# Optimization experiments

Measured on AMD Instinct MI355X. Metric: run time of the kernel, lower is better.

The kernel has to match this reference:

```python
import jax, jax.numpy as jnp
import numpy as np

N = 65536   # total nodes
E = 1048576 # total edges (avg degree 16)
B = 512     # graphs in batch
H = 4       # gat1 heads
C = 64      # per-head channels / GNN_HIDDEN


def segment_softmax(logits, seg, num_segments):
    # numerically stable softmax over segments (PyG softmax semantics, eps=1e-16)
    m = jax.ops.segment_max(logits, seg, num_segments=num_segments)
    m = jnp.where(jnp.isfinite(m), m, 0.0)
    e = jnp.exp(logits - m[seg])
    s = jax.ops.segment_sum(e, seg, num_segments=num_segments)
    return e / (s[seg] + 1e-16)


def gat_conv(x, edge_index, edge_attr, W, att_src, att_dst, We, att_edge, bias, heads, out_ch, concat):
    # PyG GATConv with edge_dim, add_self_loops=False
    n = x.shape[0]
    h = (x @ W).reshape(n, heads, out_ch)                 # (N,H,C)
    src, dst = edge_index[0], edge_index[1]
    a_s = jnp.sum(h * att_src, axis=-1)                   # (N,H)
    a_d = jnp.sum(h * att_dst, axis=-1)                   # (N,H)
    he = (edge_attr @ We).reshape(-1, heads, out_ch)      # (E,H,C)
    a_e = jnp.sum(he * att_edge, axis=-1)                 # (E,H)
    alpha = jax.nn.leaky_relu(a_s[src] + a_d[dst] + a_e, negative_slope=0.2)
    alpha = segment_softmax(alpha, dst, n)                # softmax over incoming edges per dst
    out = jax.ops.segment_sum(h[src] * alpha[..., None], dst, num_segments=n)  # (N,H,C)
    out = out.reshape(n, heads * out_ch) if concat else out.mean(axis=1)
    return out + bias


def setup_inputs() -> dict:
    key = jax.random.key(0)
    ks = jax.random.split(key, 24)
    s = 0.05
    d = {}
    d["global_feat"] = jax.random.normal(ks[0], (B, 512), jnp.float32)
    d["x"] = jax.random.normal(ks[1], (N, 13), jnp.float32)
    d["roi_feats"] = jax.random.normal(ks[2], (N, 256), jnp.float32)
    d["edge_index"] = jax.random.randint(ks[3], (2, E), 0, N)
    d["edge_attr"] = jax.random.normal(ks[4], (E, 5), jnp.float32)
    d["batch_vec"] = jnp.sort(jax.random.randint(ks[5], (N,), 0, B))
    # roi_proj / scene_proj
    d["roi_W"] = jax.random.normal(ks[6], (256, 64), jnp.float32) * s
    d["roi_b"] = jnp.zeros((64,), jnp.float32)
    d["scene_W"] = jax.random.normal(ks[7], (512, 128), jnp.float32) * s
    d["scene_b"] = jnp.zeros((128,), jnp.float32)
    d["g1_W"] = jax.random.normal(ks[8], (77, H * C), jnp.float32) * s
    d["g1_att_src"] = jax.random.normal(ks[9], (H, C), jnp.float32) * s
    d["g1_att_dst"] = jax.random.normal(ks[10], (H, C), jnp.float32) * s
    d["g1_We"] = jax.random.normal(ks[11], (5, H * C), jnp.float32) * s
    d["g1_att_edge"] = jax.random.normal(ks[12], (H, C), jnp.float32) * s
    d["g1_bias"] = jnp.zeros((H * C,), jnp.float32)
    # gat2: 256 -> 64, 1 head
    d["g2_W"] = jax.random.normal(ks[13], (H * C, C), jnp.float32) * s
    d["g2_att_src"] = jax.random.normal(ks[14], (1, C), jnp.float32) * s
    d["g2_att_dst"] = jax.random.normal(ks[15], (1, C), jnp.float32) * s
    d["g2_We"] = jax.random.normal(ks[16], (5, C), jnp.float32) * s
    d["g2_att_edge"] = jax.random.normal(ks[17], (1, C), jnp.float32) * s
    d["g2_bias"] = jnp.zeros((C,), jnp.float32)
    # attention pooling gate + classifier
    d["gate_W"] = jax.random.normal(ks[18], (C, 1), jnp.float32) * s
    d["gate_b"] = jnp.zeros((1,), jnp.float32)
    d["cls1_W"] = jax.random.normal(ks[19], (128 + C, 64), jnp.float32) * s
    d["cls1_b"] = jnp.zeros((64,), jnp.float32)
    d["cls2_W"] = jax.random.normal(ks[20], (64, 3), jnp.float32) * s
    d["cls2_b"] = jnp.zeros((3,), jnp.float32)
    return d


def reference(global_feat, x, roi_feats, edge_index, edge_attr, batch_vec,
              roi_W, roi_b, scene_W, scene_b,
              g1_W, g1_att_src, g1_att_dst, g1_We, g1_att_edge, g1_bias,
              g2_W, g2_att_src, g2_att_dst, g2_We, g2_att_edge, g2_bias,
              gate_W, gate_b, cls1_W, cls1_b, cls2_W, cls2_b):
    scene = global_feat @ scene_W + scene_b                       # (B,128)
    vis = jax.nn.relu(roi_feats @ roi_W + roi_b)                  # (N,64)
    h = jnp.concatenate([x, vis], axis=-1)                        # (N,77)
    h = jax.nn.relu(gat_conv(h, edge_index, edge_attr, g1_W, g1_att_src, g1_att_dst, g1_We, g1_att_edge, g1_bias, H, C, True))
    h = gat_conv(h, edge_index, edge_attr, g2_W, g2_att_src, g2_att_dst, g2_We, g2_att_edge, g2_bias, 1, C, False)  # (N,64)
    # GlobalAttention pooling
    gate = segment_softmax((h @ gate_W + gate_b)[:, 0], batch_vec, B)
    rel = jax.ops.segment_sum(gate[:, None] * h, batch_vec, num_segments=B)  # (B,64)
    comb = jnp.concatenate([scene, rel], axis=-1)                 # (B,192)
    hid = jax.nn.relu(comb @ cls1_W + cls1_b)                     # dropout off (eval)
    return hid @ cls2_W + cls2_b                                  # (B,3)
```

## Files before the change

kernel.cpp:

```cpp
#include <hip/hip_runtime.h>

#define N_NODES 65536
#define N_EDGES 1048576
#define NB      512

typedef unsigned short u16;
typedef unsigned int   u32;
typedef unsigned long long u64;

typedef __attribute__((ext_vector_type(8))) short bf16x8;
typedef __attribute__((ext_vector_type(4))) float f32x4;

__device__ __forceinline__ float bf2f(u16 u) { return __uint_as_float(((u32)u) << 16); }
__device__ __forceinline__ float lo16(u32 u) { return __uint_as_float(u << 16); }
__device__ __forceinline__ float hi16(u32 u) { return __uint_as_float(u & 0xffff0000u); }
__device__ __forceinline__ u16 f2bf(float f) {
    u32 u = __float_as_uint(f);
    u32 r = (u + 0x7fffu + ((u >> 16) & 1u)) >> 16;
    return (u16)r;
}
__device__ __forceinline__ u32 pk2(float a, float b) {
    return (u32)f2bf(a) | ((u32)f2bf(b) << 16);
}
__device__ __forceinline__ float wsum(float v) {
    for (int o = 32; o; o >>= 1) v += __shfl_xor(v, o, 64);
    return v;
}
__device__ __forceinline__ float wmax(float v) {
    for (int o = 32; o; o >>= 1) v = fmaxf(v, __shfl_xor(v, o, 64));
    return v;
}

__global__ __launch_bounds__(512) void k_wprep(const float* __restrict__ g1W, const float* __restrict__ roiW,
                                               const float* __restrict__ g2W,
                                               const float* __restrict__ g1We, const float* __restrict__ g1ae,
                                               const float* __restrict__ g2We, const float* __restrict__ g2ae,
                                               u16* __restrict__ g1Wt, u16* __restrict__ roiWt,
                                               u16* __restrict__ g2Wt, float* __restrict__ M1,
                                               float* __restrict__ M2) {
    int b = blockIdx.x, t = threadIdx.x;
    if (b < 48) {
        int idx = b * 512 + t;
        int c = idx / 96, k = idx - 96 * c;
        float v = 0.f;
        if (k < 77) {
            int ko = (k < 64) ? (13 + k) : (k - 64);
            v = g1W[(size_t)ko * 256 + c];
        }
        g1Wt[idx] = f2bf(v);
    } else if (b < 80) {
        int idx = (b - 48) * 512 + t;
        int c = idx >> 8, k = idx & 255;
        roiWt[idx] = f2bf(roiW[(size_t)k * 64 + c]);
    } else if (b < 112) {
        int idx = (b - 80) * 512 + t;
        int c = idx >> 8, k = idx & 255;
        g2Wt[idx] = f2bf(g2W[(size_t)k * 64 + c]);
    } else {
        if (t < 20) {
            int j = t >> 2, h = t & 3;
            float s = 0.f;
            for (int c = 0; c < 64; c++) s += g1We[j * 256 + h * 64 + c] * g1ae[h * 64 + c];
            M1[t] = s;
        } else if (t < 25) {
            int j = t - 20;
            float s = 0.f;
            for (int c = 0; c < 64; c++) s += g2We[j * 64 + c] * g2ae[c];
            M2[j] = s;
        }
    }
}

__global__ __launch_bounds__(256) void k_scene(const float* __restrict__ gf, const float* __restrict__ W,
                                               const float* __restrict__ bias, float* __restrict__ scene) {
    int idx = blockIdx.x * 256 + threadIdx.x;
    int b = idx >> 7, j = idx & 127;
    float acc = 0.f;
    for (int k = 0; k < 512; k++) acc += gf[b * 512 + k] * W[k * 128 + j];
    scene[idx] = acc + bias[j];
}

__global__ __launch_bounds__(256) void k_hist(const int* ei, int* cnt) {
    int e = blockIdx.x * 256 + threadIdx.x;
    atomicAdd(&cnt[ei[N_EDGES + e]], 1);
}

__global__ __launch_bounds__(256) void k_scan_blk(const int* __restrict__ cnt, int* __restrict__ pre,
                                                  int* __restrict__ bsum) {
    __shared__ int sd[256];
    int t = threadIdx.x, b = blockIdx.x;
    int base = b * 1024 + t * 4;
    int4 c = *(const int4*)(cnt + base);
    int s = c.x + c.y + c.z + c.w;
    sd[t] = s;
    __syncthreads();
    for (int off = 1; off < 256; off <<= 1) {
        int v = (t >= off) ? sd[t - off] : 0;
        __syncthreads();
        sd[t] += v;
        __syncthreads();
    }
    int excl = sd[t] - s;
    int4 p;
    p.x = excl;
    p.y = excl + c.x;
    p.z = excl + c.x + c.y;
    p.w = excl + c.x + c.y + c.z;
    *(int4*)(pre + base) = p;
    if (t == 255) bsum[b] = sd[255];
}

__global__ __launch_bounds__(64) void k_scan_top(int* bsum) {
    int t = threadIdx.x;
    int v = bsum[t];
    int inc = v;
    for (int off = 1; off < 64; off <<= 1) {
        int u = __shfl_up(inc, off, 64);
        if (t >= off) inc += u;
    }
    bsum[t] = inc - v;
}

__global__ __launch_bounds__(256) void k_scan_fix(const int* __restrict__ pre, const int* __restrict__ bsum,
                                                  int* __restrict__ row_ptr, int* __restrict__ coarse_cur) {
    int i = blockIdx.x * 256 + threadIdx.x;
    int v = pre[i] + bsum[i >> 10];
    row_ptr[i] = v;
    if ((i & 255) == 0) coarse_cur[i >> 8] = v;
    if (i == 0) row_ptr[N_NODES] = N_EDGES;
}

__global__ __launch_bounds__(256) void k_bucket(const int* __restrict__ ei, int* coarse_cur,
                                                u32* __restrict__ bpack, int* __restrict__ bsrc) {
    __shared__ u32 stageP[2048];
    __shared__ int stageS[2048];
    __shared__ int bcnt[256], bscan[256], boff[256], gbase[256];
    int t = threadIdx.x;
    int e0 = blockIdx.x * 2048;
    bcnt[t] = 0;
    __syncthreads();
    int dreg[8], sreg[8];
    for (int it = 0; it < 8; it++) {
        int e = e0 + it * 256 + t;
        int dd = ei[N_EDGES + e];
        dreg[it] = dd;
        sreg[it] = ei[e];
        atomicAdd(&bcnt[dd >> 8], 1);
    }
    __syncthreads();
    int v = bcnt[t];
    bscan[t] = v;
    __syncthreads();
    for (int off = 1; off < 256; off <<= 1) {
        int u = (t >= off) ? bscan[t - off] : 0;
        __syncthreads();
        bscan[t] += u;
        __syncthreads();
    }
    boff[t] = bscan[t] - v;
    gbase[t] = v ? atomicAdd(&coarse_cur[t], v) : 0;
    __syncthreads();
    for (int it = 0; it < 8; it++) {
        int e = e0 + it * 256 + t;
        int b = dreg[it] >> 8;
        int pos = atomicAdd(&boff[b], 1);
        stageP[pos] = ((u32)e << 12) | (u32)(dreg[it] & 255);
        stageS[pos] = sreg[it];
    }
    __syncthreads();
    for (int idx = t; idx < 2048; idx += 256) {
        int lo = 0, hi = 255;
        while (lo < hi) { int mid = (lo + hi) >> 1; if (bscan[mid] > idx) hi = mid; else lo = mid + 1; }
        int b = lo;
        int g = gbase[b] + (idx - (bscan[b] - bcnt[b]));
        bpack[g] = stageP[idx];
        bsrc[g] = stageS[idx];
    }
}

__global__ __launch_bounds__(256) void k_sortp(const u32* __restrict__ bpack, const int* __restrict__ bsrc,
                                               const int* __restrict__ row_ptr, const float* __restrict__ ea,
                                               const float* __restrict__ M1, const float* __restrict__ M2,
                                               int* __restrict__ ssrc, float* __restrict__ a1es,
                                               float* __restrict__ a2es) {
    __shared__ int cur[256];
    int t = threadIdx.x, b = blockIdx.x;
    int nbase = b * 256;
    cur[t] = row_ptr[nbase + t];
    __syncthreads();
    float m1[20], m2[5];
    #pragma unroll
    for (int j = 0; j < 20; j++) m1[j] = M1[j];
    #pragma unroll
    for (int j = 0; j < 5; j++) m2[j] = M2[j];
    int beg = row_ptr[nbase];
    int end = row_ptr[nbase + 256];
    for (int i = beg + t; i < end; i += 256) {
        u32 wd = bpack[i];
        int src = bsrc[i];
        int d8 = wd & 255;
        int e = (int)(wd >> 12);
        int pos = atomicAdd(&cur[d8], 1);
        ssrc[pos] = src;
        const float* ep = ea + (size_t)e * 5;
        float v0 = ep[0], v1 = ep[1], v2 = ep[2], v3 = ep[3], v4 = ep[4];
        float4 o;
        o.x = v0*m1[0]  + v1*m1[4]  + v2*m1[8]  + v3*m1[12] + v4*m1[16];
        o.y = v0*m1[1]  + v1*m1[5]  + v2*m1[9]  + v3*m1[13] + v4*m1[17];
        o.z = v0*m1[2]  + v1*m1[6]  + v2*m1[10] + v3*m1[14] + v4*m1[18];
        o.w = v0*m1[3]  + v1*m1[7]  + v2*m1[11] + v3*m1[15] + v4*m1[19];
        *(float4*)(a1es + (size_t)pos * 4) = o;
        a2es[pos] = v0*m2[0] + v1*m2[1] + v2*m2[2] + v3*m2[3] + v4*m2[4];
    }
}

__global__ __launch_bounds__(256) void k_vis(const float* __restrict__ roi, const u16* __restrict__ Wt,
                                             const float* __restrict__ bias, u16* __restrict__ out) {
    __shared__ u16 At[64][264];
    int t = threadIdx.x;
    int w = t >> 6, l = t & 63, lo = l & 15, hi = l >> 4;
    int n0 = blockIdx.x * 64;
    int r = t >> 2, sub = t & 3;
    const float* rp = roi + (size_t)(n0 + r) * 256 + sub * 4;
    #pragma unroll
    for (int q = 0; q < 16; q++) {
        float4 v = *(const float4*)(rp + q * 16);
        uint2 p;
        p.x = pk2(v.x, v.y);
        p.y = pk2(v.z, v.w);
        *(uint2*)&At[r][q * 16 + sub * 4] = p;
    }
    float bb[4][4];
    #pragma unroll
    for (int cb = 0; cb < 4; cb++)
        #pragma unroll
        for (int rg = 0; rg < 4; rg++) bb[cb][rg] = bias[cb * 16 + hi * 4 + rg];
    __syncthreads();
    f32x4 acc[4];
    #pragma unroll
    for (int cb = 0; cb < 4; cb++) acc[cb] = (f32x4){0.f, 0.f, 0.f, 0.f};
    #pragma unroll
    for (int ks = 0; ks < 8; ks++) {
        bf16x8 af = *(const bf16x8*)(&At[w * 16 + lo][ks * 32 + hi * 8]);
        #pragma unroll
        for (int cb = 0; cb < 4; cb++) {
            bf16x8 wf = *(const bf16x8*)(Wt + (size_t)(cb * 16 + lo) * 256 + ks * 32 + hi * 8);
            acc[cb] = __builtin_amdgcn_mfma_f32_16x16x32_bf16(wf, af, acc[cb], 0, 0, 0);
        }
    }
    int nrow = n0 + w * 16 + lo;
    #pragma unroll
    for (int cb = 0; cb < 4; cb++) {
        uint2 p;
        p.x = pk2(fmaxf(acc[cb][0] + bb[cb][0], 0.f), fmaxf(acc[cb][1] + bb[cb][1], 0.f));
        p.y = pk2(fmaxf(acc[cb][2] + bb[cb][2], 0.f), fmaxf(acc[cb][3] + bb[cb][3], 0.f));
        *(uint2*)(out + (size_t)nrow * 64 + cb * 16 + hi * 4) = p;
    }
}

__global__ __launch_bounds__(256) void k_h1(const float* __restrict__ x, const u16* __restrict__ vis,
                                            const u16* __restrict__ Wt,
                                            const float* __restrict__ as_, const float* __restrict__ ad_,
                                            u16* __restrict__ h1, float* __restrict__ a1s,
                                            float* __restrict__ a1d) {
    __shared__ u16 At[64][104];
    int t = threadIdx.x;
    int w = t >> 6, l = t & 63, lo = l & 15, hi = l >> 4;
    int n0 = blockIdx.x * 64;
    int r = t >> 2, sub = t & 3;
    {
        const uint4* vp = (const uint4*)(vis + (size_t)(n0 + r) * 64 + sub * 16);
        uint4 v0 = vp[0], v1 = vp[1];
        *(uint4*)&At[r][sub * 16] = v0;
        *(uint4*)&At[r][sub * 16 + 8] = v1;
        if (sub == 0) {
            const float* xp = x + (size_t)(n0 + r) * 13;
            #pragma unroll
            for (int j = 0; j < 13; j++) At[r][64 + j] = f2bf(xp[j]);
        } else if (sub == 1) {
            #pragma unroll
            for (int j = 77; j < 96; j++) At[r][j] = 0;
        }
    }
    bf16x8 wf[4][3];
    float asv[4][4], adv[4][4];
    #pragma unroll
    for (int cb = 0; cb < 4; cb++) {
        #pragma unroll
        for (int ks = 0; ks < 3; ks++)
            wf[cb][ks] = *(const bf16x8*)(Wt + (size_t)(w * 64 + cb * 16 + lo) * 96 + ks * 32 + hi * 8);
        #pragma unroll
        for (int rg = 0; rg < 4; rg++) {
            asv[cb][rg] = as_[w * 64 + cb * 16 + hi * 4 + rg];
            adv[cb][rg] = ad_[w * 64 + cb * 16 + hi * 4 + rg];
        }
    }
    __syncthreads();
    #pragma unroll
    for (int nb = 0; nb < 4; nb++) {
        f32x4 acc[4];
        #pragma unroll
        for (int cb = 0; cb < 4; cb++) acc[cb] = (f32x4){0.f, 0.f, 0.f, 0.f};
        #pragma unroll
        for (int ks = 0; ks < 3; ks++) {
            bf16x8 af = *(const bf16x8*)(&At[nb * 16 + lo][ks * 32 + hi * 8]);
            #pragma unroll
            for (int cb = 0; cb < 4; cb++)
                acc[cb] = __builtin_amdgcn_mfma_f32_16x16x32_bf16(wf[cb][ks], af, acc[cb], 0, 0, 0);
        }
        int nrow = n0 + nb * 16 + lo;
        float ps = 0.f, pd = 0.f;
        #pragma unroll
        for (int cb = 0; cb < 4; cb++) {
            uint2 p;
            p.x = pk2(acc[cb][0], acc[cb][1]);
            p.y = pk2(acc[cb][2], acc[cb][3]);
            *(uint2*)(h1 + (size_t)nrow * 256 + w * 64 + cb * 16 + hi * 4) = p;
            ps += acc[cb][0] * asv[cb][0] + acc[cb][1] * asv[cb][1]
                + acc[cb][2] * asv[cb][2] + acc[cb][3] * asv[cb][3];
            pd += acc[cb][0] * adv[cb][0] + acc[cb][1] * adv[cb][1]
                + acc[cb][2] * adv[cb][2] + acc[cb][3] * adv[cb][3];
        }
        ps += __shfl_xor(ps, 16, 64); ps += __shfl_xor(ps, 32, 64);
        pd += __shfl_xor(pd, 16, 64); pd += __shfl_xor(pd, 32, 64);
        if (hi == 0) {
            a1s[nrow * 4 + w] = ps;
            a1d[nrow * 4 + w] = pd;
        }
    }
}

__global__ __launch_bounds__(256) void k_sg1(const int* __restrict__ row_ptr, const int* __restrict__ ssrc,
                                             const float* __restrict__ a1s, const float* __restrict__ a1d,
                                             const float* __restrict__ a1es, const u16* __restrict__ h1,
                                             const float* __restrict__ bias, u16* __restrict__ out1) {
    __shared__ float wl[4][1024];
    __shared__ int   sl[4][256];
    int t = threadIdx.x;
    int wv = t >> 6, L = t & 63;
    int n = blockIdx.x * 4 + wv;
    int beg = row_ptr[n], deg = row_ptr[n + 1] - beg;
    int lim = (deg < 256) ? deg : 256;
    {
        int h = L >> 4, j = L & 15;
        float adn = a1d[n * 4 + h];
        float m = -3.0e38f, s = 0.f;
        for (int i = j; i < deg; i += 16) {
            int pos = beg + i;
            int sv = ssrc[pos];
            if (h == 0 && i < 256) sl[wv][i] = sv;
            float l = a1s[sv * 4 + h] + adn + a1es[(size_t)pos * 4 + h];
            l = (l > 0.f) ? l : 0.2f * l;
            if (i < 256) wl[wv][i * 4 + h] = l;
            if (l > m) { s = s * __expf(m - l) + 1.f; m = l; }
            else       { s += __expf(l - m); }
        }
        for (int o = 1; o < 16; o <<= 1) {
            float mo = __shfl_xor(m, o, 64), so = __shfl_xor(s, o, 64);
            float M = fmaxf(m, mo);
            s = s * __expf(m - M) + so * __expf(mo - M);
            m = M;
        }
        float inv = 1.f / (s + 1e-16f);
        for (int i = j; i < lim; i += 16)
            wl[wv][i * 4 + h] = __expf(wl[wv][i * 4 + h] - m) * inv;
    }
    asm volatile("" ::: "memory");
    __builtin_amdgcn_s_waitcnt(0);
    int halfE = L >> 5;
    int L32 = L & 31;
    int hd = L32 >> 3;
    float acc[8];
    #pragma unroll
    for (int j = 0; j < 8; j++) acc[j] = 0.f;
    uint4 U[4];
    float W[4];
    #pragma unroll
    for (int k = 0; k < 4; k++) {
        int ii = 2 * k + halfE;
        bool v = ii < deg;
        int s = v ? sl[wv][ii] : 0;
        W[k] = v ? wl[wv][ii * 4 + hd] : 0.f;
        U[k] = *((const uint4*)(h1 + (size_t)s * 256) + L32);
    }
    for (int i = 0; i < deg; i += 8) {
        uint4 C0 = U[0], C1 = U[1], C2 = U[2], C3 = U[3];
        float W0 = W[0], W1 = W[1], W2 = W[2], W3 = W[3];
        int ib = i + 8;
        #pragma unroll
        for (int k = 0; k < 4; k++) {
            int ii = ib + 2 * k + halfE;
            bool v = ii < deg;
            int s = v ? sl[wv][ii] : 0;
            W[k] = v ? wl[wv][ii * 4 + hd] : 0.f;
            U[k] = *((const uint4*)(h1 + (size_t)s * 256) + L32);
        }
        acc[0] += W0 * lo16(C0.x) + W1 * lo16(C1.x) + W2 * lo16(C2.x) + W3 * lo16(C3.x);
        acc[1] += W0 * hi16(C0.x) + W1 * hi16(C1.x) + W2 * hi16(C2.x) + W3 * hi16(C3.x);
        acc[2] += W0 * lo16(C0.y) + W1 * lo16(C1.y) + W2 * lo16(C2.y) + W3 * lo16(C3.y);
        acc[3] += W0 * hi16(C0.y) + W1 * hi16(C1.y) + W2 * hi16(C2.y) + W3 * hi16(C3.y);
        acc[4] += W0 * lo16(C0.z) + W1 * lo16(C1.z) + W2 * lo16(C2.z) + W3 * lo16(C3.z);
        acc[5] += W0 * hi16(C0.z) + W1 * hi16(C1.z) + W2 * hi16(C2.z) + W3 * hi16(C3.z);
        acc[6] += W0 * lo16(C0.w) + W1 * lo16(C1.w) + W2 * lo16(C2.w) + W3 * lo16(C3.w);
        acc[7] += W0 * hi16(C0.w) + W1 * hi16(C1.w) + W2 * hi16(C2.w) + W3 * hi16(C3.w);
    }
    #pragma unroll
    for (int j = 0; j < 8; j++) acc[j] += __shfl_xor(acc[j], 32, 64);
    if (halfE == 0) {
        float4 b0 = *(const float4*)(bias + 8 * L32);
        float4 b1 = *(const float4*)(bias + 8 * L32 + 4);
        uint4 pk;
        pk.x = (u32)f2bf(fmaxf(acc[0] + b0.x, 0.f)) | ((u32)f2bf(fmaxf(acc[1] + b0.y, 0.f)) << 16);
        pk.y = (u32)f2bf(fmaxf(acc[2] + b0.z, 0.f)) | ((u32)f2bf(fmaxf(acc[3] + b0.w, 0.f)) << 16);
        pk.z = (u32)f2bf(fmaxf(acc[4] + b1.x, 0.f)) | ((u32)f2bf(fmaxf(acc[5] + b1.y, 0.f)) << 16);
        pk.w = (u32)f2bf(fmaxf(acc[6] + b1.z, 0.f)) | ((u32)f2bf(fmaxf(acc[7] + b1.w, 0.f)) << 16);
        *((uint4*)(out1 + (size_t)n * 256) + L32) = pk;
    }
}

__global__ __launch_bounds__(256) void k_h2(const u16* __restrict__ A, const u16* __restrict__ Wt,
                                            const float* __restrict__ as_, const float* __restrict__ ad_,
                                            u16* __restrict__ out, float* __restrict__ a2s,
                                            float* __restrict__ a2d) {
    int t = threadIdx.x;
    int w = t >> 6, l = t & 63, lo = l & 15, hi = l >> 4;
    int nrow = blockIdx.x * 64 + w * 16 + lo;
    f32x4 acc[4];
    #pragma unroll
    for (int cb = 0; cb < 4; cb++) acc[cb] = (f32x4){0.f, 0.f, 0.f, 0.f};
    const u16* ap = A + (size_t)nrow * 256 + hi * 8;
    #pragma unroll
    for (int ks = 0; ks < 8; ks++) {
        bf16x8 af = *(const bf16x8*)(ap + ks * 32);
        #pragma unroll
        for (int cb = 0; cb < 4; cb++) {
            bf16x8 wf = *(const bf16x8*)(Wt + (size_t)(cb * 16 + lo) * 256 + ks * 32 + hi * 8);
            acc[cb] = __builtin_amdgcn_mfma_f32_16x16x32_bf16(wf, af, acc[cb], 0, 0, 0);
        }
    }
    float ps = 0.f, pd = 0.f;
    #pragma unroll
    for (int cb = 0; cb < 4; cb++) {
        uint2 p;
        p.x = pk2(acc[cb][0], acc[cb][1]);
        p.y = pk2(acc[cb][2], acc[cb][3]);
        *(uint2*)(out + (size_t)nrow * 64 + cb * 16 + hi * 4) = p;
        #pragma unroll
        for (int rg = 0; rg < 4; rg++) {
            float a = acc[cb][rg];
            ps += a * as_[cb * 16 + hi * 4 + rg];
            pd += a * ad_[cb * 16 + hi * 4 + rg];
        }
    }
    ps += __shfl_xor(ps, 16, 64); ps += __shfl_xor(ps, 32, 64);
    pd += __shfl_xor(pd, 16, 64); pd += __shfl_xor(pd, 32, 64);
    if (hi == 0) {
        a2s[nrow] = ps;
        a2d[nrow] = pd;
    }
}

__global__ __launch_bounds__(256) void k_sg2(const int* __restrict__ row_ptr, const int* __restrict__ ssrc,
                                             const float* __restrict__ a2s, const float* __restrict__ a2d,
                                             const float* __restrict__ a2es, const u16* __restrict__ h2b,
                                             const float* __restrict__ bias, float* __restrict__ hfin) {
    __shared__ float wl[4][256];
    __shared__ int   sl[4][256];
    int t = threadIdx.x;
    int wv = t >> 6, L = t & 63;
    int n = blockIdx.x * 4 + wv;
    int beg = row_ptr[n], deg = row_ptr[n + 1] - beg;
    int lim = (deg < 256) ? deg : 256;
    {
        float adn = a2d[n];
        float m = -3.0e38f, s = 0.f;
        for (int i = L; i < deg; i += 64) {
            int pos = beg + i;
            int sv = ssrc[pos];
            if (i < 256) sl[wv][i] = sv;
            float l = a2s[sv] + adn + a2es[pos];
            l = (l > 0.f) ? l : 0.2f * l;
            if (i < 256) wl[wv][i] = l;
            if (l > m) { s = s * __expf(m - l) + 1.f; m = l; }
            else       { s += __expf(l - m); }
        }
        for (int o = 1; o < 64; o <<= 1) {
            float mo = __shfl_xor(m, o, 64), so = __shfl_xor(s, o, 64);
            float M = fmaxf(m, mo);
            s = s * __expf(m - M) + so * __expf(mo - M);
            m = M;
        }
        float inv = 1.f / (s + 1e-16f);
        for (int i = L; i < lim; i += 64)
            wl[wv][i] = __expf(wl[wv][i] - m) * inv;
    }
    asm volatile("" ::: "memory");
    __builtin_amdgcn_s_waitcnt(0);
    int halfE = L >> 5;
    int L32 = L & 31;
    float a0 = 0.f, a1v = 0.f;
    const u32* h2u = (const u32*)h2b;
    u32 U[4];
    float W[4];
    #pragma unroll
    for (int k = 0; k < 4; k++) {
        int ii = 2 * k + halfE;
        bool v = ii < deg;
        int s = v ? sl[wv][ii] : 0;
        W[k] = v ? wl[wv][ii] : 0.f;
        U[k] = h2u[(size_t)s * 32 + L32];
    }
    for (int i = 0; i < deg; i += 8) {
        u32 C0 = U[0], C1 = U[1], C2 = U[2], C3 = U[3];
        float W0 = W[0], W1 = W[1], W2 = W[2], W3 = W[3];
        int ib = i + 8;
        #pragma unroll
        for (int k = 0; k < 4; k++) {
            int ii = ib + 2 * k + halfE;
            bool v = ii < deg;
            int s = v ? sl[wv][ii] : 0;
            W[k] = v ? wl[wv][ii] : 0.f;
            U[k] = h2u[(size_t)s * 32 + L32];
        }
        a0  += W0 * lo16(C0) + W1 * lo16(C1) + W2 * lo16(C2) + W3 * lo16(C3);
        a1v += W0 * hi16(C0) + W1 * hi16(C1) + W2 * hi16(C2) + W3 * hi16(C3);
    }
    a0  += __shfl_xor(a0, 32, 64);
    a1v += __shfl_xor(a1v, 32, 64);
    if (halfE == 0) {
        float2 o;
        o.x = a0  + bias[2 * L32];
        o.y = a1v + bias[2 * L32 + 1];
        *(float2*)(hfin + (size_t)n * 64 + 2 * L32) = o;
    }
}

__global__ __launch_bounds__(64) void k_pool(const int* __restrict__ bvec, const float* __restrict__ hf,
                                             const float* gateW, const float* gateb,
                                             const float* __restrict__ scene,
                                             const float* c1W, const float* c1b,
                                             const float* c2W, const float* c2b,
                                             float* __restrict__ outp) {
    int b = blockIdx.x, lane = threadIdx.x;
    __shared__ float gwl[64], se[64], comb[192], hid[64];
    gwl[lane] = gateW[lane];
    __syncthreads();
    int s0, s1;
    { int lo = 0, hi = N_NODES; while (lo < hi) { int mid = (lo + hi) >> 1; if (bvec[mid] < b) lo = mid + 1; else hi = mid; } s0 = lo; }
    { int lo = 0, hi = N_NODES; while (lo < hi) { int mid = (lo + hi) >> 1; if (bvec[mid] < b + 1) lo = mid + 1; else hi = mid; } s1 = lo; }
    float gb = gateb[0];
    float m = -3.0e38f, ssum = 0.f, acc = 0.f;
    for (int cs = s0; cs < s1; cs += 64) {
        int cnt = min(64, s1 - cs);
        float l = -3.0e38f;
        if (lane < cnt) {
            int n = cs + lane;
            float d = 0.f;
            for (int i = 0; i < 64; i++) d += hf[(size_t)n * 64 + i] * gwl[i];
            l = d + gb;
        }
        float cm = wmax(l);
        float newm = fmaxf(m, cm);
        float rsc = __expf(m - newm);
        float e = (lane < cnt) ? __expf(l - newm) : 0.f;
        float es = wsum(e);
        ssum = ssum * rsc + es;
        se[lane] = e;
        __syncthreads();
        float a2 = 0.f;
        for (int i = 0; i < cnt; i++) a2 += se[i] * hf[(size_t)(cs + i) * 64 + lane];
        acc = acc * rsc + a2;
        __syncthreads();
        m = newm;
    }
    float rel = acc / (ssum + 1e-16f);
    comb[lane] = scene[b * 128 + lane];
    comb[64 + lane] = scene[b * 128 + 64 + lane];
    comb[128 + lane] = rel;
    __syncthreads();
    float hj = 0.f;
    for (int k = 0; k < 192; k++) hj += comb[k] * c1W[k * 64 + lane];
    hj += c1b[lane];
    hid[lane] = fmaxf(hj, 0.f);
    __syncthreads();
    if (lane < 3) {
        float o = 0.f;
        for (int k = 0; k < 64; k++) o += hid[k] * c2W[k * 3 + lane];
        o += c2b[lane];
        outp[b * 3 + lane] = o;
    }
}

extern "C" void kernel_launch(void* const* d_in, const int* in_sizes, int n_in,
                              void* d_out, int out_size, void* d_ws, size_t ws_size,
                              hipStream_t stream) {
    (void)in_sizes; (void)n_in; (void)out_size; (void)ws_size;
    const float* gf     = (const float*)d_in[0];
    const float* x      = (const float*)d_in[1];
    const float* roi    = (const float*)d_in[2];
    const int*   ei     = (const int*)d_in[3];
    const float* ea     = (const float*)d_in[4];
    const int*   bvec   = (const int*)d_in[5];
    const float* roiW   = (const float*)d_in[6];
    const float* roib   = (const float*)d_in[7];
    const float* sceneW = (const float*)d_in[8];
    const float* sceneb = (const float*)d_in[9];
    const float* g1W    = (const float*)d_in[10];
    const float* g1as   = (const float*)d_in[11];
    const float* g1ad   = (const float*)d_in[12];
    const float* g1We   = (const float*)d_in[13];
    const float* g1ae   = (const float*)d_in[14];
    const float* g1b    = (const float*)d_in[15];
    const float* g2W    = (const float*)d_in[16];
    const float* g2as   = (const float*)d_in[17];
    const float* g2ad   = (const float*)d_in[18];
    const float* g2We   = (const float*)d_in[19];
    const float* g2ae   = (const float*)d_in[20];
    const float* g2b    = (const float*)d_in[21];
    const float* gateW  = (const float*)d_in[22];
    const float* gateb  = (const float*)d_in[23];
    const float* c1W    = (const float*)d_in[24];
    const float* c1b    = (const float*)d_in[25];
    const float* c2W    = (const float*)d_in[26];
    const float* c2b    = (const float*)d_in[27];

    char* w = (char*)d_ws;
    size_t o = 0;
    auto nxt = [&](size_t bytes) -> char* {
        char* p = w + o;
        o += (bytes + 255) & ~(size_t)255;
        return p;
    };
    float* scene  = (float*)nxt((size_t)NB * 128 * 4);
    float* M1     = (float*)nxt(80);
    float* M2     = (float*)nxt(32);
    u16* g1Wt     = (u16*)nxt((size_t)256 * 96 * 2);
    u16* roiWt    = (u16*)nxt((size_t)64 * 256 * 2);
    u16* g2Wt     = (u16*)nxt((size_t)64 * 256 * 2);
    int* cnt      = (int*)nxt((size_t)N_NODES * 4);
    int* pre      = (int*)nxt((size_t)N_NODES * 4);
    int* bsum     = (int*)nxt(64 * 4);
    int* row_ptr  = (int*)nxt((size_t)(N_NODES + 1) * 4);
    int* coarse   = (int*)nxt(256 * 4);
    u32* bpack    = (u32*)nxt((size_t)N_EDGES * 4);
    int* bsrc     = (int*)nxt((size_t)N_EDGES * 4);
    int* ssrc     = (int*)nxt((size_t)N_EDGES * 4);
    float* a1es   = (float*)nxt((size_t)N_EDGES * 16);
    float* a2es   = (float*)nxt((size_t)N_EDGES * 4);
    u16* visb     = (u16*)nxt((size_t)N_NODES * 64 * 2);
    u16* h1       = (u16*)nxt((size_t)N_NODES * 256 * 2);
    u16* out1     = (u16*)nxt((size_t)N_NODES * 256 * 2);
    u16* h2b      = (u16*)nxt((size_t)N_NODES * 64 * 2);
    float* hfin   = (float*)nxt((size_t)N_NODES * 64 * 4);
    float* a1s    = (float*)nxt((size_t)N_NODES * 16);
    float* a1d    = (float*)nxt((size_t)N_NODES * 16);
    float* a2s    = (float*)nxt((size_t)N_NODES * 4);
    float* a2d    = (float*)nxt((size_t)N_NODES * 4);

    hipMemsetAsync(cnt, 0, (size_t)N_NODES * 4, stream);
    k_wprep<<<113, 512, 0, stream>>>(g1W, roiW, g2W, g1We, g1ae, g2We, g2ae,
                                     g1Wt, roiWt, g2Wt, M1, M2);
    k_scene<<<(NB * 128) / 256, 256, 0, stream>>>(gf, sceneW, sceneb, scene);
    k_hist<<<N_EDGES / 256, 256, 0, stream>>>(ei, cnt);
    k_scan_blk<<<64, 256, 0, stream>>>(cnt, pre, bsum);
    k_scan_top<<<1, 64, 0, stream>>>(bsum);
    k_scan_fix<<<N_NODES / 256, 256, 0, stream>>>(pre, bsum, row_ptr, coarse);
    k_bucket<<<512, 256, 0, stream>>>(ei, coarse, bpack, bsrc);
    k_sortp<<<256, 256, 0, stream>>>(bpack, bsrc, row_ptr, ea, M1, M2, ssrc, a1es, a2es);
    k_vis<<<N_NODES / 64, 256, 0, stream>>>(roi, roiWt, roib, visb);
    k_h1<<<N_NODES / 64, 256, 0, stream>>>(x, visb, g1Wt, g1as, g1ad, h1, a1s, a1d);
    k_sg1<<<N_NODES / 4, 256, 0, stream>>>(row_ptr, ssrc, a1s, a1d, a1es, h1, g1b, out1);
    k_h2<<<N_NODES / 64, 256, 0, stream>>>(out1, g2Wt, g2as, g2ad, h2b, a2s, a2d);
    k_sg2<<<N_NODES / 4, 256, 0, stream>>>(row_ptr, ssrc, a2s, a2d, a2es, h2b, g2b, hfin);
    k_pool<<<NB, 64, 0, stream>>>(bvec, hfin, gateW, gateb, scene, c1W, c1b, c2W, c2b, (float*)d_out);
}
```

Measured before the change: 538.4 us.

## Fuse ROI projection into GAT1 linear, deepen gather prefetch, enlarge bucket tiles

Merges the ROI projection kernel into the first GAT linear kernel, so the vis activations stay in shared memory and no longer make a round trip through global memory. The edge aggregation kernels drop the shared source-index cache, read ssrc directly, and prefetch eight neighbor rows instead of four to keep more gathers in flight. The bucket kernel handles 4096 edges per block instead of 2048, which halves the block count and the global atomics but uses more shared memory. The risk is more register pressure in the aggregation loops and lower occupancy in the bucket kernel.

```diff
diff --git a/kernel.cpp b/kernel.cpp
--- a/kernel.cpp
+++ b/kernel.cpp
@@ -132,15 +132,15 @@
 
 __global__ __launch_bounds__(256) void k_bucket(const int* __restrict__ ei, int* coarse_cur,
                                                 u32* __restrict__ bpack, int* __restrict__ bsrc) {
-    __shared__ u32 stageP[2048];
-    __shared__ int stageS[2048];
+    __shared__ u32 stageP[4096];
+    __shared__ int stageS[4096];
     __shared__ int bcnt[256], bscan[256], boff[256], gbase[256];
     int t = threadIdx.x;
-    int e0 = blockIdx.x * 2048;
+    int e0 = blockIdx.x * 4096;
     bcnt[t] = 0;
     __syncthreads();
-    int dreg[8], sreg[8];
-    for (int it = 0; it < 8; it++) {
+    int dreg[16], sreg[16];
+    for (int it = 0; it < 16; it++) {
         int e = e0 + it * 256 + t;
         int dd = ei[N_EDGES + e];
         dreg[it] = dd;
@@ -160,7 +160,7 @@
     boff[t] = bscan[t] - v;
     gbase[t] = v ? atomicAdd(&coarse_cur[t], v) : 0;
     __syncthreads();
-    for (int it = 0; it < 8; it++) {
+    for (int it = 0; it < 16; it++) {
         int e = e0 + it * 256 + t;
         int b = dreg[it] >> 8;
         int pos = atomicAdd(&boff[b], 1);
@@ -168,7 +168,7 @@
         stageS[pos] = sreg[it];
     }
     __syncthreads();
-    for (int idx = t; idx < 2048; idx += 256) {
+    for (int idx = t; idx < 4096; idx += 256) {
         int lo = 0, hi = 255;
         while (lo < hi) { int mid = (lo + hi) >> 1; if (bscan[mid] > idx) hi = mid; else lo = mid + 1; }
         int b = lo;
@@ -214,9 +214,14 @@
     }
 }
 
-__global__ __launch_bounds__(256) void k_vis(const float* __restrict__ roi, const u16* __restrict__ Wt,
-                                             const float* __restrict__ bias, u16* __restrict__ out) {
+__global__ __launch_bounds__(256) void k_vh(const float* __restrict__ roi, const u16* __restrict__ WtV,
+                                            const float* __restrict__ visb, const float* __restrict__ x,
+                                            const u16* __restrict__ Wt1,
+                                            const float* __restrict__ as_, const float* __restrict__ ad_,
+                                            u16* __restrict__ h1, float* __restrict__ a1s,
+                                            float* __restrict__ a1d) {
     __shared__ u16 At[64][264];
+    __shared__ u16 A1[64][104];
     int t = threadIdx.x;
     int w = t >> 6, l = t & 63, lo = l & 15, hi = l >> 4;
     int n0 = blockIdx.x * 64;
@@ -230,65 +235,48 @@
         p.y = pk2(v.z, v.w);
         *(uint2*)&At[r][q * 16 + sub * 4] = p;
     }
+    if (sub == 0) {
+        const float* xp = x + (size_t)(n0 + r) * 13;
+        #pragma unroll
+        for (int j = 0; j < 13; j++) A1[r][64 + j] = f2bf(xp[j]);
+    } else if (sub == 1) {
+        #pragma unroll
+        for (int j = 77; j < 96; j++) A1[r][j] = 0;
+    }
     float bb[4][4];
     #pragma unroll
     for (int cb = 0; cb < 4; cb++)
         #pragma unroll
-        for (int rg = 0; rg < 4; rg++) bb[cb][rg] = bias[cb * 16 + hi * 4 + rg];
-    __syncthreads();
-    f32x4 acc[4];
-    #pragma unroll
-    for (int cb = 0; cb < 4; cb++) acc[cb] = (f32x4){0.f, 0.f, 0.f, 0.f};
-    #pragma unroll
-    for (int ks = 0; ks < 8; ks++) {
-        bf16x8 af = *(const bf16x8*)(&At[w * 16 + lo][ks * 32 + hi * 8]);
+        for (int rg = 0; rg < 4; rg++) bb[cb][rg] = visb[cb * 16 + hi * 4 + rg];
+    __syncthreads();
+    {
+        f32x4 acc[4];
+        #pragma unroll
+        for (int cb = 0; cb < 4; cb++) acc[cb] = (f32x4){0.f, 0.f, 0.f, 0.f};
+        #pragma unroll
+        for (int ks = 0; ks < 8; ks++) {
+            bf16x8 af = *(const bf16x8*)(&At[w * 16 + lo][ks * 32 + hi * 8]);
+            #pragma unroll
+            for (int cb = 0; cb < 4; cb++) {
+                bf16x8 wf = *(const bf16x8*)(WtV + (size_t)(cb * 16 + lo) * 256 + ks * 32 + hi * 8);
+                acc[cb] = __builtin_amdgcn_mfma_f32_16x16x32_bf16(wf, af, acc[cb], 0, 0, 0);
+            }
+        }
         #pragma unroll
         for (int cb = 0; cb < 4; cb++) {
-            bf16x8 wf = *(const bf16x8*)(Wt + (size_t)(cb * 16 + lo) * 256 + ks * 32 + hi * 8);
-            acc[cb] = __builtin_amdgcn_mfma_f32_16x16x32_bf16(wf, af, acc[cb], 0, 0, 0);
-        }
-    }
-    int nrow = n0 + w * 16 + lo;
+            uint2 p;
+            p.x = pk2(fmaxf(acc[cb][0] + bb[cb][0], 0.f), fmaxf(acc[cb][1] + bb[cb][1], 0.f));
+            p.y = pk2(fmaxf(acc[cb][2] + bb[cb][2], 0.f), fmaxf(acc[cb][3] + bb[cb][3], 0.f));
+            *(uint2*)&A1[w * 16 + lo][cb * 16 + hi * 4] = p;
+        }
+    }
+    bf16x8 wf1[4][3];
+    float asv[4][4], adv[4][4];
     #pragma unroll
     for (int cb = 0; cb < 4; cb++) {
-        uint2 p;
-        p.x = pk2(fmaxf(acc[cb][0] + bb[cb][0], 0.f), fmaxf(acc[cb][1] + bb[cb][1], 0.f));
-        p.y = pk2(fmaxf(acc[cb][2] + bb[cb][2], 0.f), fmaxf(acc[cb][3] + bb[cb][3], 0.f));
-        *(uint2*)(out + (size_t)nrow * 64 + cb * 16 + hi * 4) = p;
-    }
-}
-
-__global__ __launch_bounds__(256) void k_h1(const float* __restrict__ x, const u16* __restrict__ vis,
-                                            const u16* __restrict__ Wt,
-                                            const float* __restrict__ as_, const float* __restrict__ ad_,
-                                            u16* __restrict__ h1, float* __restrict__ a1s,
-                                            float* __restrict__ a1d) {
-    __shared__ u16 At[64][104];
-    int t = threadIdx.x;
-    int w = t >> 6, l = t & 63, lo = l & 15, hi = l >> 4;
-    int n0 = blockIdx.x * 64;
-    int r = t >> 2, sub = t & 3;
-    {
-        const uint4* vp = (const uint4*)(vis + (size_t)(n0 + r) * 64 + sub * 16);
-        uint4 v0 = vp[0], v1 = vp[1];
-        *(uint4*)&At[r][sub * 16] = v0;
-        *(uint4*)&At[r][sub * 16 + 8] = v1;
-        if (sub == 0) {
-            const float* xp = x + (size_t)(n0 + r) * 13;
-            #pragma unroll
-            for (int j = 0; j < 13; j++) At[r][64 + j] = f2bf(xp[j]);
-        } else if (sub == 1) {
-            #pragma unroll
-            for (int j = 77; j < 96; j++) At[r][j] = 0;
-        }
-    }
-    bf16x8 wf[4][3];
-    float asv[4][4], adv[4][4];
-    #pragma unroll
-    for (int cb = 0; cb < 4; cb++) {
         #pragma unroll
         for (int ks = 0; ks < 3; ks++)
-            wf[cb][ks] = *(const bf16x8*)(Wt + (size_t)(w * 64 + cb * 16 + lo) * 96 + ks * 32 + hi * 8);
+            wf1[cb][ks] = *(const bf16x8*)(Wt1 + (size_t)(w * 64 + cb * 16 + lo) * 96 + ks * 32 + hi * 8);
         #pragma unroll
         for (int rg = 0; rg < 4; rg++) {
             asv[cb][rg] = as_[w * 64 + cb * 16 + hi * 4 + rg];
@@ -303,10 +291,10 @@
         for (int cb = 0; cb < 4; cb++) acc[cb] = (f32x4){0.f, 0.f, 0.f, 0.f};
         #pragma unroll
         for (int ks = 0; ks < 3; ks++) {
-            bf16x8 af = *(const bf16x8*)(&At[nb * 16 + lo][ks * 32 + hi * 8]);
+            bf16x8 af = *(const bf16x8*)(&A1[nb * 16 + lo][ks * 32 + hi * 8]);
             #pragma unroll
             for (int cb = 0; cb < 4; cb++)
-                acc[cb] = __builtin_amdgcn_mfma_f32_16x16x32_bf16(wf[cb][ks], af, acc[cb], 0, 0, 0);
+                acc[cb] = __builtin_amdgcn_mfma_f32_16x16x32_bf16(wf1[cb][ks], af, acc[cb], 0, 0, 0);
         }
         int nrow = n0 + nb * 16 + lo;
         float ps = 0.f, pd = 0.f;
@@ -335,7 +323,6 @@
                                              const float* __restrict__ a1es, const u16* __restrict__ h1,
                                              const float* __restrict__ bias, u16* __restrict__ out1) {
     __shared__ float wl[4][1024];
-    __shared__ int   sl[4][256];
     int t = threadIdx.x;
     int wv = t >> 6, L = t & 63;
     int n = blockIdx.x * 4 + wv;
@@ -347,9 +334,7 @@
         float m = -3.0e38f, s = 0.f;
         for (int i = j; i < deg; i += 16) {
             int pos = beg + i;
-            int sv = ssrc[pos];
-            if (h == 0 && i < 256) sl[wv][i] = sv;
-            float l = a1s[sv * 4 + h] + adn + a1es[(size_t)pos * 4 + h];
+            float l = a1s[ssrc[pos] * 4 + h] + adn + a1es[(size_t)pos * 4 + h];
             l = (l > 0.f) ? l : 0.2f * l;
             if (i < 256) wl[wv][i * 4 + h] = l;
             if (l > m) { s = s * __expf(m - l) + 1.f; m = l; }
@@ -373,36 +358,46 @@
     float acc[8];
     #pragma unroll
     for (int j = 0; j < 8; j++) acc[j] = 0.f;
-    uint4 U[4];
-    float W[4];
-    #pragma unroll
-    for (int k = 0; k < 4; k++) {
-        int ii = 2 * k + halfE;
+    uint4 U[8];
+    float W[8];
+    auto LD = [&](int k, int ii) {
         bool v = ii < deg;
-        int s = v ? sl[wv][ii] : 0;
-        W[k] = v ? wl[wv][ii * 4 + hd] : 0.f;
+        int iw = (ii < 255) ? ii : 255;
+        int s = v ? ssrc[beg + ii] : 0;
+        W[k] = v ? wl[wv][iw * 4 + hd] : 0.f;
         U[k] = *((const uint4*)(h1 + (size_t)s * 256) + L32);
-    }
-    for (int i = 0; i < deg; i += 8) {
-        uint4 C0 = U[0], C1 = U[1], C2 = U[2], C3 = U[3];
-        float W0 = W[0], W1 = W[1], W2 = W[2], W3 = W[3];
-        int ib = i + 8;
-        #pragma unroll
-        for (int k = 0; k < 4; k++) {
-            int ii = ib + 2 * k + halfE;
-            bool v = ii < deg;
-            int s = v ? sl[wv][ii] : 0;
-            W[k] = v ? wl[wv][ii * 4 + hd] : 0.f;
-            U[k] = *((const uint4*)(h1 + (size_t)s * 256) + L32);
-        }
-        acc[0] += W0 * lo16(C0.x) + W1 * lo16(C1.x) + W2 * lo16(C2.x) + W3 * lo16(C3.x);
-        acc[1] += W0 * hi16(C0.x) + W1 * hi16(C1.x) + W2 * hi16(C2.x) + W3 * hi16(C3.x);
-        acc[2] += W0 * lo16(C0.y) + W1 * lo16(C1.y) + W2 * lo16(C2.y) + W3 * lo16(C3.y);
-        acc[3] += W0 * hi16(C0.y) + W1 * hi16(C1.y) + W2 * hi16(C2.y) + W3 * hi16(C3.y);
-        acc[4] += W0 * lo16(C0.z) + W1 * lo16(C1.z) + W2 * lo16(C2.z) + W3 * lo16(C3.z);
-        acc[5] += W0 * hi16(C0.z) + W1 * hi16(C1.z) + W2 * hi16(C2.z) + W3 * hi16(C3.z);
-        acc[6] += W0 * lo16(C0.w) + W1 * lo16(C1.w) + W2 * lo16(C2.w) + W3 * lo16(C3.w);
-        acc[7] += W0 * hi16(C0.w) + W1 * hi16(C1.w) + W2 * hi16(C2.w) + W3 * hi16(C3.w);
+    };
+    #pragma unroll
+    for (int k = 0; k < 8; k++) LD(k, 2 * (k & 3) + halfE + (k >> 2) * 8);
+    for (int i = 0; i < deg; i += 16) {
+        {
+            uint4 C0 = U[0], C1 = U[1], C2 = U[2], C3 = U[3];
+            float W0 = W[0], W1 = W[1], W2 = W[2], W3 = W[3];
+            #pragma unroll
+            for (int k = 0; k < 4; k++) LD(k, i + 16 + 2 * k + halfE);
+            acc[0] += W0 * lo16(C0.x) + W1 * lo16(C1.x) + W2 * lo16(C2.x) + W3 * lo16(C3.x);
+            acc[1] += W0 * hi16(C0.x) + W1 * hi16(C1.x) + W2 * hi16(C2.x) + W3 * hi16(C3.x);
+            acc[2] += W0 * lo16(C0.y) + W1 * lo16(C1.y) + W2 * lo16(C2.y) + W3 * lo16(C3.y);
+            acc[3] += W0 * hi16(C0.y) + W1 * hi16(C1.y) + W2 * hi16(C2.y) + W3 * hi16(C3.y);
+            acc[4] += W0 * lo16(C0.z) + W1 * lo16(C1.z) + W2 * lo16(C2.z) + W3 * lo16(C3.z);
+            acc[5] += W0 * hi16(C0.z) + W1 * hi16(C1.z) + W2 * hi16(C2.z) + W3 * hi16(C3.z);
+            acc[6] += W0 * lo16(C0.w) + W1 * lo16(C1.w) + W2 * lo16(C2.w) + W3 * lo16(C3.w);
+            acc[7] += W0 * hi16(C0.w) + W1 * hi16(C1.w) + W2 * hi16(C2.w) + W3 * hi16(C3.w);
+        }
+        {
+            uint4 C0 = U[4], C1 = U[5], C2 = U[6], C3 = U[7];
+            float W0 = W[4], W1 = W[5], W2 = W[6], W3 = W[7];
+            #pragma unroll
+            for (int k = 0; k < 4; k++) LD(4 + k, i + 24 + 2 * k + halfE);
+            acc[0] += W0 * lo16(C0.x) + W1 * lo16(C1.x) + W2 * lo16(C2.x) + W3 * lo16(C3.x);
+            acc[1] += W0 * hi16(C0.x) + W1 * hi16(C1.x) + W2 * hi16(C2.x) + W3 * hi16(C3.x);
+            acc[2] += W0 * lo16(C0.y) + W1 * lo16(C1.y) + W2 * lo16(C2.y) + W3 * lo16(C3.y);
+            acc[3] += W0 * hi16(C0.y) + W1 * hi16(C1.y) + W2 * hi16(C2.y) + W3 * hi16(C3.y);
+            acc[4] += W0 * lo16(C0.z) + W1 * lo16(C1.z) + W2 * lo16(C2.z) + W3 * lo16(C3.z);
+            acc[5] += W0 * hi16(C0.z) + W1 * hi16(C1.z) + W2 * hi16(C2.z) + W3 * hi16(C3.z);
+            acc[6] += W0 * lo16(C0.w) + W1 * lo16(C1.w) + W2 * lo16(C2.w) + W3 * lo16(C3.w);
+            acc[7] += W0 * hi16(C0.w) + W1 * hi16(C1.w) + W2 * hi16(C2.w) + W3 * hi16(C3.w);
+        }
     }
     #pragma unroll
     for (int j = 0; j < 8; j++) acc[j] += __shfl_xor(acc[j], 32, 64);
@@ -465,7 +460,6 @@
                                              const float* __restrict__ a2es, const u16* __restrict__ h2b,
                                              const float* __restrict__ bias, float* __restrict__ hfin) {
     __shared__ float wl[4][256];
-    __shared__ int   sl[4][256];
     int t = threadIdx.x;
     int wv = t >> 6, L = t & 63;
     int n = blockIdx.x * 4 + wv;
@@ -476,9 +470,7 @@
         float m = -3.0e38f, s = 0.f;
         for (int i = L; i < deg; i += 64) {
             int pos = beg + i;
-            int sv = ssrc[pos];
-            if (i < 256) sl[wv][i] = sv;
-            float l = a2s[sv] + adn + a2es[pos];
+            float l = a2s[ssrc[pos]] + adn + a2es[pos];
             l = (l > 0.f) ? l : 0.2f * l;
             if (i < 256) wl[wv][i] = l;
             if (l > m) { s = s * __expf(m - l) + 1.f; m = l; }
@@ -500,30 +492,34 @@
     int L32 = L & 31;
     float a0 = 0.f, a1v = 0.f;
     const u32* h2u = (const u32*)h2b;
-    u32 U[4];
-    float W[4];
-    #pragma unroll
-    for (int k = 0; k < 4; k++) {
-        int ii = 2 * k + halfE;
+    u32 U[8];
+    float W[8];
+    auto LD = [&](int k, int ii) {
         bool v = ii < deg;
-        int s = v ? sl[wv][ii] : 0;
-        W[k] = v ? wl[wv][ii] : 0.f;
+        int iw = (ii < 255) ? ii : 255;
+        int s = v ? ssrc[beg + ii] : 0;
+        W[k] = v ? wl[wv][iw] : 0.f;
         U[k] = h2u[(size_t)s * 32 + L32];
-    }
-    for (int i = 0; i < deg; i += 8) {
-        u32 C0 = U[0], C1 = U[1], C2 = U[2], C3 = U[3];
-        float W0 = W[0], W1 = W[1], W2 = W[2], W3 = W[3];
-        int ib = i + 8;
-        #pragma unroll
-        for (int k = 0; k < 4; k++) {
-            int ii = ib + 2 * k + halfE;
-            bool v = ii < deg;
-            int s = v ? sl[wv][ii] : 0;
-            W[k] = v ? wl[wv][ii] : 0.f;
-            U[k] = h2u[(size_t)s * 32 + L32];
-        }
-        a0  += W0 * lo16(C0) + W1 * lo16(C1) + W2 * lo16(C2) + W3 * lo16(C3);
-        a1v += W0 * hi16(C0) + W1 * hi16(C1) + W2 * hi16(C2) + W3 * hi16(C3);
+    };
+    #pragma unroll
+    for (int k = 0; k < 8; k++) LD(k, 2 * (k & 3) + halfE + (k >> 2) * 8);
+    for (int i = 0; i < deg; i += 16) {
+        {
+            u32 C0 = U[0], C1 = U[1], C2 = U[2], C3 = U[3];
+            float W0 = W[0], W1 = W[1], W2 = W[2], W3 = W[3];
+            #pragma unroll
+            for (int k = 0; k < 4; k++) LD(k, i + 16 + 2 * k + halfE);
+            a0  += W0 * lo16(C0) + W1 * lo16(C1) + W2 * lo16(C2) + W3 * lo16(C3);
+            a1v += W0 * hi16(C0) + W1 * hi16(C1) + W2 * hi16(C2) + W3 * hi16(C3);
+        }
+        {
+            u32 C0 = U[4], C1 = U[5], C2 = U[6], C3 = U[7];
+            float W0 = W[4], W1 = W[5], W2 = W[6], W3 = W[7];
+            #pragma unroll
+            for (int k = 0; k < 4; k++) LD(4 + k, i + 24 + 2 * k + halfE);
+            a0  += W0 * lo16(C0) + W1 * lo16(C1) + W2 * lo16(C2) + W3 * lo16(C3);
+            a1v += W0 * hi16(C0) + W1 * hi16(C1) + W2 * hi16(C2) + W3 * hi16(C3);
+        }
     }
     a0  += __shfl_xor(a0, 32, 64);
     a1v += __shfl_xor(a1v, 32, 64);
@@ -647,7 +643,6 @@
     int* ssrc     = (int*)nxt((size_t)N_EDGES * 4);
     float* a1es   = (float*)nxt((size_t)N_EDGES * 16);
     float* a2es   = (float*)nxt((size_t)N_EDGES * 4);
-    u16* visb     = (u16*)nxt((size_t)N_NODES * 64 * 2);
     u16* h1       = (u16*)nxt((size_t)N_NODES * 256 * 2);
     u16* out1     = (u16*)nxt((size_t)N_NODES * 256 * 2);
     u16* h2b      = (u16*)nxt((size_t)N_NODES * 64 * 2);
@@ -665,10 +660,9 @@
     k_scan_blk<<<64, 256, 0, stream>>>(cnt, pre, bsum);
     k_scan_top<<<1, 64, 0, stream>>>(bsum);
     k_scan_fix<<<N_NODES / 256, 256, 0, stream>>>(pre, bsum, row_ptr, coarse);
-    k_bucket<<<512, 256, 0, stream>>>(ei, coarse, bpack, bsrc);
+    k_bucket<<<256, 256, 0, stream>>>(ei, coarse, bpack, bsrc);
     k_sortp<<<256, 256, 0, stream>>>(bpack, bsrc, row_ptr, ea, M1, M2, ssrc, a1es, a2es);
-    k_vis<<<N_NODES / 64, 256, 0, stream>>>(roi, roiWt, roib, visb);
-    k_h1<<<N_NODES / 64, 256, 0, stream>>>(x, visb, g1Wt, g1as, g1ad, h1, a1s, a1d);
+    k_vh<<<N_NODES / 64, 256, 0, stream>>>(roi, roiWt, roib, x, g1Wt, g1as, g1ad, h1, a1s, a1d);
     k_sg1<<<N_NODES / 4, 256, 0, stream>>>(row_ptr, ssrc, a1s, a1d, a1es, h1, g1b, out1);
     k_h2<<<N_NODES / 64, 256, 0, stream>>>(out1, g2Wt, g2as, g2ad, h2b, a2s, a2d);
     k_sg2<<<N_NODES / 4, 256, 0, stream>>>(row_ptr, ssrc, a2s, a2d, a2es, h2b, g2b, hfin);
```

Measured after the change: 602.1 us. 1.12x slower.
